# Kernel optimization log

Hardware: AMD Instinct MI355X
Metric: run time of the kernel (lower is better)

## Reference

```python
import jax, jax.numpy as jnp
import numpy as np

D_MODEL = 1024
NUM_HEADS = 16
D_HEAD = D_MODEL // NUM_HEADS
THETA = 10000.0


def _apply_rope(x, pos):
    # x: [B, H, S, Dh]; pos: [S]
    inv_freq = 1.0 / (THETA ** (jnp.arange(0, D_HEAD, 2, dtype=jnp.float32) / D_HEAD))  # [Dh/2]
    freqs = pos[:, None].astype(x.dtype) * inv_freq.astype(x.dtype)  # [S, Dh/2]
    cos = jnp.cos(freqs)  # [S, Dh/2]
    sin = jnp.sin(freqs)
    x1 = x[..., 0::2]  # [B, H, S, Dh/2]
    x2 = x[..., 1::2]
    even = x1 * cos - x2 * sin
    odd = x1 * sin + x2 * cos
    # interleave back: stack on last axis then flatten
    out = jnp.stack([even, odd], axis=-1).reshape(x.shape)
    return out


def setup_inputs() -> dict:
    key = jax.random.key(0)
    k0, k1, k2, k3, k4 = jax.random.split(key, 5)
    B, S = 2, 2048
    scale = 0.02
    return {
        "in_features": jax.random.normal(k0, (B, S, D_MODEL), dtype=jnp.float32),
        "Wq": jax.random.normal(k1, (D_MODEL, D_MODEL), dtype=jnp.float32) * scale,
        "Wk": jax.random.normal(k2, (D_MODEL, D_MODEL), dtype=jnp.float32) * scale,
        "Wv": jax.random.normal(k3, (D_MODEL, D_MODEL), dtype=jnp.float32) * scale,
        "Wo": jax.random.normal(k4, (D_MODEL, D_MODEL), dtype=jnp.float32) * scale,
    }


def reference(in_features, Wq, Wk, Wv, Wo):
    B, S, _ = in_features.shape
    H, Dh = NUM_HEADS, D_HEAD

    def proj(W):
        # torch Linear: y = x @ W^T; split heads -> [B, H, S, Dh]
        y = jnp.einsum('bsd,ed->bse', in_features, W)
        return y.reshape(B, S, H, Dh).transpose(0, 2, 1, 3)

    q = proj(Wq)
    k = proj(Wk)
    v = proj(Wv)

    pos = jnp.arange(S)
    q = _apply_rope(q, pos)
    k = _apply_rope(k, pos)

    scores = jnp.einsum('bhqd,bhkd->bhqk', q, k) / jnp.sqrt(jnp.asarray(Dh, q.dtype))
    causal = jnp.tril(jnp.ones((S, S), dtype=bool))  # True = keep
    scores = jnp.where(causal[None, None, :, :], scores, -jnp.inf)
    att = jax.nn.softmax(scores, axis=-1)
    out = jnp.einsum('bhqk,bhkd->bhqd', att, v)  # [B, H, S, Dh]
    out = out.transpose(0, 2, 1, 3).reshape(B, S, H * Dh)
    return jnp.einsum('bsd,ed->bse', out, Wo)
```

## Files before the change

### kernel.cpp

```cpp
#include <hip/hip_runtime.h>
#include <hip/hip_bf16.h>
#include <math.h>

#define D_MODEL 1024
#define NHEAD 16
#define DHEAD 64
#define SEQ 2048
#define BATCH 2
#define MTOT (BATCH * SEQ)

typedef __attribute__((ext_vector_type(8))) short bf16x8;
typedef __attribute__((ext_vector_type(4))) float f32x4;

static __device__ __forceinline__ ushort f2b(float x) {
  __hip_bfloat16 h = __float2bfloat16(x);
  union { __hip_bfloat16 h; ushort u; } cv; cv.h = h; return cv.u;
}
static __device__ __forceinline__ float b2f(ushort u) {
  union { ushort u; __hip_bfloat16 h; } cv; cv.u = u; return __bfloat162float(cv.h);
}

#define GLLDS16(gp, lp)                                                     \
  __builtin_amdgcn_global_load_lds(                                         \
      (const __attribute__((address_space(1))) unsigned int*)(gp),          \
      (__attribute__((address_space(3))) unsigned int*)(lp), 16, 0, 0)

__global__ __launch_bounds__(256)
void f2b_x(const float* __restrict__ in, ushort* __restrict__ out) {
  int i = blockIdx.x * 256 + threadIdx.x;
  float4 v = ((const float4*)in)[i];
  ushort4 o;
  o.x = f2b(v.x); o.y = f2b(v.y); o.z = f2b(v.z); o.w = f2b(v.w);
  ((ushort4*)out)[i] = o;
}

__global__ __launch_bounds__(256)
void f2b_w4(const float* __restrict__ Wq, const float* __restrict__ Wk,
            const float* __restrict__ Wv, const float* __restrict__ Wo,
            ushort* __restrict__ oq, ushort* __restrict__ ok,
            ushort* __restrict__ ov, ushort* __restrict__ oo) {
  int z = blockIdx.y;
  const float* in = (z == 0) ? Wq : (z == 1) ? Wk : (z == 2) ? Wv : Wo;
  ushort* out = (z == 0) ? oq : (z == 1) ? ok : (z == 2) ? ov : oo;
  int i = blockIdx.x * 256 + threadIdx.x;
  float4 v = ((const float4*)in)[i];
  ushort4 o;
  o.x = f2b(v.x); o.y = f2b(v.y); o.z = f2b(v.z); o.w = f2b(v.w);
  ((ushort4*)out)[i] = o;
}

__global__ __launch_bounds__(256)
void gemm_bf16(const ushort* __restrict__ A,
               const ushort* __restrict__ W0, const ushort* __restrict__ W1,
               const ushort* __restrict__ W2,
               float* __restrict__ outF,
               ushort* __restrict__ o0, ushort* __restrict__ o1,
               ushort* __restrict__ o2, int mode) {
  __shared__ ushort As[128 * 32];
  __shared__ ushort Bs[128 * 32];
  const int tid = threadIdx.x;
  const int lane = tid & 63, w = tid >> 6;
  const int quad = lane >> 4, l15 = lane & 15;
  const int wy = w >> 1, wx = w & 1;
  const int m0 = blockIdx.y * 128, n0 = blockIdx.x * 128;
  const int z = blockIdx.z;
  const ushort* W = (z == 0) ? W0 : (z == 1) ? W1 : W2;
  ushort* outB = (z == 0) ? o0 : (z == 1) ? o1 : o2;

  const int r0 = tid >> 2, c0 = tid & 3;
  const int gc = c0 ^ (r0 & 3);
  const ushort* Ag0 = A + (size_t)(m0 + r0) * D_MODEL + gc * 8;
  const ushort* Ag1 = A + (size_t)(m0 + r0 + 64) * D_MODEL + gc * 8;
  const ushort* Wg0 = W + (size_t)(n0 + r0) * D_MODEL + gc * 8;
  const ushort* Wg1 = W + (size_t)(n0 + r0 + 64) * D_MODEL + gc * 8;

  const int sw = quad ^ (l15 & 3);

  f32x4 acc[4][4];
#pragma unroll
  for (int i = 0; i < 4; ++i)
#pragma unroll
    for (int j = 0; j < 4; ++j) acc[i][j] = (f32x4){0.f, 0.f, 0.f, 0.f};

  for (int kt = 0; kt < D_MODEL / 32; ++kt) {
    if (kt) __syncthreads();
    GLLDS16(Ag0 + kt * 32, &As[(size_t)tid * 8]);
    GLLDS16(Ag1 + kt * 32, &As[(size_t)(tid + 256) * 8]);
    GLLDS16(Wg0 + kt * 32, &Bs[(size_t)tid * 8]);
    GLLDS16(Wg1 + kt * 32, &Bs[(size_t)(tid + 256) * 8]);
    __syncthreads();

    bf16x8 af[4], bfr[4];
#pragma unroll
    for (int mt = 0; mt < 4; ++mt) {
      int row = wy * 64 + mt * 16 + l15;
      af[mt] = *(const bf16x8*)&As[(row * 4 + sw) * 8];
    }
#pragma unroll
    for (int nt = 0; nt < 4; ++nt) {
      int row = wx * 64 + nt * 16 + l15;
      bfr[nt] = *(const bf16x8*)&Bs[(row * 4 + sw) * 8];
    }
#pragma unroll
    for (int mt = 0; mt < 4; ++mt)
#pragma unroll
      for (int nt = 0; nt < 4; ++nt)
        acc[mt][nt] = __builtin_amdgcn_mfma_f32_16x16x32_bf16(
            af[mt], bfr[nt], acc[mt][nt], 0, 0, 0);
  }

#pragma unroll
  for (int mt = 0; mt < 4; ++mt) {
#pragma unroll
    for (int r = 0; r < 4; ++r) {
      int m = m0 + wy * 64 + mt * 16 + quad * 4 + r;
#pragma unroll
      for (int nt = 0; nt < 4; ++nt) {
        int n = n0 + wx * 64 + nt * 16 + l15;
        float v = acc[mt][nt][r];
        if (mode == 0) {
          outF[(size_t)m * D_MODEL + n] = v;
        } else {
          int b = m >> 11, s = m & (SEQ - 1);
          int h = n >> 6, dh = n & 63;
          outB[(((size_t)(b * NHEAD + h)) * SEQ + s) * DHEAD + dh] = f2b(v);
        }
      }
    }
  }
}

__global__ __launch_bounds__(256)
void rope_b(ushort* __restrict__ Q, ushort* __restrict__ K) {
  int p = blockIdx.x * 256 + threadIdx.x;
  ushort* ptr = (blockIdx.y == 0 ? Q : K) + 2 * (size_t)p;
  int i = p & 31;
  int s = (p >> 5) & (SEQ - 1);
  float inv = exp2f((float)i * -0.4152410118609203f);
  float f = (float)s * inv;
  float sn, cs;
  sincosf(f, &sn, &cs);
  uint v = *(uint*)ptr;
  float x1 = b2f((ushort)(v & 0xFFFF));
  float x2 = b2f((ushort)(v >> 16));
  float e = x1 * cs - x2 * sn;
  float o = x1 * sn + x2 * cs;
  *(uint*)ptr = (uint)f2b(e) | ((uint)f2b(o) << 16);
}

__global__ __launch_bounds__(256)
void vtrans(const ushort* __restrict__ V, ushort* __restrict__ Vt) {
  __shared__ ushort T[64][72];
  int bh = blockIdx.y;
  int s0 = blockIdx.x * 64;
  int t = threadIdx.x;
  int r = t >> 2, c4 = t & 3;
  const ushort* src = V + ((size_t)bh * SEQ + s0 + r) * 64 + c4 * 16;
  *(float4*)&T[r][c4 * 16]     = *(const float4*)(src);
  *(float4*)&T[r][c4 * 16 + 8] = *(const float4*)(src + 8);
  __syncthreads();
  union { ushort u[16]; float4 f[2]; } tmp;
#pragma unroll
  for (int j = 0; j < 16; ++j) tmp.u[j] = T[c4 * 16 + j][r];
  ushort* dst = Vt + ((size_t)bh * 64 + r) * SEQ + s0 + c4 * 16;
  *(float4*)dst = tmp.f[0];
  *(float4*)(dst + 8) = tmp.f[1];
}

__global__ __launch_bounds__(256)
void flash_mfma(const ushort* __restrict__ Q, const ushort* __restrict__ K,
                const ushort* __restrict__ Vt, ushort* __restrict__ O) {
  __shared__ ushort Ks[64][72];
  __shared__ ushort Vs[64][72];
  __shared__ ushort Ps[4][16][72];
  const int tid = threadIdx.x;
  const int lane = tid & 63, w = tid >> 6;
  const int quad = lane >> 4, l15 = lane & 15;
  const int h = blockIdx.y, b = blockIdx.z;
  const int qt = (h >= 8) ? (31 - blockIdx.x) : blockIdx.x;
  const int bh = b * NHEAD + h;

  const ushort* Qrow = Q + ((size_t)bh * SEQ + qt * 64 + w * 16 + l15) * 64;
  bf16x8 aq0 = *(const bf16x8*)(Qrow + quad * 8);
  bf16x8 aq1 = *(const bf16x8*)(Qrow + 32 + quad * 8);

  const int sr = tid >> 3, sc8 = (tid & 7) * 8;
  const ushort* Kg0 = K + ((size_t)bh * SEQ + sr) * 64 + sc8;
  const ushort* Kg1 = Kg0 + (size_t)32 * 64;
  const ushort* Vg0 = Vt + ((size_t)bh * 64 + sr) * SEQ + sc8;
  const ushort* Vg1 = Vg0 + (size_t)32 * SEQ;

  float rsl[4];
  f32x4 accO[4];
#pragma unroll
  for (int r = 0; r < 4; ++r) rsl[r] = 0.f;
#pragma unroll
  for (int nt = 0; nt < 4; ++nt) accO[nt] = (f32x4){0.f, 0.f, 0.f, 0.f};

  float4 pk0 = *(const float4*)(Kg0);
  float4 pk1 = *(const float4*)(Kg1);
  float4 pv0 = *(const float4*)(Vg0);
  float4 pv1 = *(const float4*)(Vg1);

  const float SCL = 0.18033688011112042f;
  const int qrow0 = qt * 64 + w * 16 + quad * 4;

  for (int kt = 0; kt <= qt; ++kt) {
    __syncthreads();
    *(float4*)&Ks[sr][sc8]      = pk0;
    *(float4*)&Ks[sr + 32][sc8] = pk1;
    *(float4*)&Vs[sr][sc8]      = pv0;
    *(float4*)&Vs[sr + 32][sc8] = pv1;
    __syncthreads();
    if (kt < qt) {
      pk0 = *(const float4*)(Kg0 + (size_t)(kt + 1) * 64 * 64);
      pk1 = *(const float4*)(Kg1 + (size_t)(kt + 1) * 64 * 64);
      pv0 = *(const float4*)(Vg0 + (kt + 1) * 64);
      pv1 = *(const float4*)(Vg1 + (kt + 1) * 64);
    }

    f32x4 sc[4];
#pragma unroll
    for (int nt = 0; nt < 4; ++nt) {
      bf16x8 bk0 = *(const bf16x8*)&Ks[nt * 16 + l15][quad * 8];
      bf16x8 bk1 = *(const bf16x8*)&Ks[nt * 16 + l15][32 + quad * 8];
      f32x4 zz = (f32x4){0.f, 0.f, 0.f, 0.f};
      zz = __builtin_amdgcn_mfma_f32_16x16x32_bf16(aq0, bk0, zz, 0, 0, 0);
      zz = __builtin_amdgcn_mfma_f32_16x16x32_bf16(aq1, bk1, zz, 0, 0, 0);
      sc[nt] = zz;
    }

    const bool diag = (kt == qt);
#pragma unroll
    for (int nt = 0; nt < 4; ++nt) {
      int kg = kt * 64 + nt * 16 + l15;
#pragma unroll
      for (int r = 0; r < 4; ++r) {
        float p = __builtin_amdgcn_exp2f(sc[nt][r] * SCL);
        if (diag && kg > qrow0 + r) p = 0.f;
        Ps[w][quad * 4 + r][nt * 16 + l15] = f2b(p);
        rsl[r] += p;
      }
    }

    bf16x8 ap0 = *(const bf16x8*)&Ps[w][l15][quad * 8];
    bf16x8 ap1 = *(const bf16x8*)&Ps[w][l15][32 + quad * 8];
#pragma unroll
    for (int nt = 0; nt < 4; ++nt) {
      bf16x8 bv0 = *(const bf16x8*)&Vs[nt * 16 + l15][quad * 8];
      bf16x8 bv1 = *(const bf16x8*)&Vs[nt * 16 + l15][32 + quad * 8];
      accO[nt] = __builtin_amdgcn_mfma_f32_16x16x32_bf16(ap0, bv0, accO[nt], 0, 0, 0);
      accO[nt] = __builtin_amdgcn_mfma_f32_16x16x32_bf16(ap1, bv1, accO[nt], 0, 0, 0);
    }
  }

#pragma unroll
  for (int r = 0; r < 4; ++r) {
#pragma unroll
    for (int off = 1; off < 16; off <<= 1) rsl[r] += __shfl_xor(rsl[r], off);
  }

#pragma unroll
  for (int r = 0; r < 4; ++r) {
    float invl = 1.f / rsl[r];
    int qrow = qt * 64 + w * 16 + quad * 4 + r;
    size_t base = ((size_t)(b * SEQ + qrow)) * D_MODEL + h * 64;
#pragma unroll
    for (int nt = 0; nt < 4; ++nt)
      O[base + nt * 16 + l15] = f2b(accO[nt][r] * invl);
  }
}

extern "C" void kernel_launch(void* const* d_in, const int* in_sizes, int n_in,
                              void* d_out, int out_size, void* d_ws, size_t ws_size,
                              hipStream_t stream) {
  const float* X  = (const float*)d_in[0];
  const float* Wq = (const float*)d_in[1];
  const float* Wk = (const float*)d_in[2];
  const float* Wv = (const float*)d_in[3];
  const float* Wo = (const float*)d_in[4];
  float* out = (float*)d_out;

  ushort* Xb  = (ushort*)d_ws;
  ushort* Wqb = Xb  + (size_t)MTOT * D_MODEL;
  ushort* Wkb = Wqb + (size_t)D_MODEL * D_MODEL;
  ushort* Wvb = Wkb + (size_t)D_MODEL * D_MODEL;
  ushort* Wob = Wvb + (size_t)D_MODEL * D_MODEL;
  ushort* Qw  = Wob + (size_t)D_MODEL * D_MODEL;
  ushort* Kw  = Qw  + (size_t)MTOT * D_MODEL;
  ushort* Vw  = Kw  + (size_t)MTOT * D_MODEL;
  ushort* Vtw = Vw  + (size_t)MTOT * D_MODEL;
  ushort* At  = Vtw + (size_t)MTOT * D_MODEL;

  f2b_x<<<(MTOT * D_MODEL / 4) / 256, 256, 0, stream>>>(X, Xb);
  f2b_w4<<<dim3((D_MODEL * D_MODEL / 4) / 256, 4), 256, 0, stream>>>(
      Wq, Wk, Wv, Wo, Wqb, Wkb, Wvb, Wob);

  gemm_bf16<<<dim3(D_MODEL / 128, MTOT / 128, 3), 256, 0, stream>>>(
      Xb, Wqb, Wkb, Wvb, nullptr, Qw, Kw, Vw, 1);

  int pairs = BATCH * NHEAD * SEQ * (DHEAD / 2);
  rope_b<<<dim3(pairs / 256, 2), 256, 0, stream>>>(Qw, Kw);

  vtrans<<<dim3(SEQ / 64, BATCH * NHEAD), 256, 0, stream>>>(Vw, Vtw);

  flash_mfma<<<dim3(SEQ / 64, NHEAD, BATCH), 256, 0, stream>>>(Qw, Kw, Vtw, At);

  gemm_bf16<<<dim3(D_MODEL / 128, MTOT / 128, 1), 256, 0, stream>>>(
      At, Wob, nullptr, nullptr, out, nullptr, nullptr, nullptr, 0);
}
```

Before: 198.4 us.

## Fuse RoPE and softmax scale into QKV GEMM epilogue, use direct LDS loads in attention

Applies RoPE and the softmax log2 scale to Q and K inside the QKV projection GEMM epilogue, using lane shuffles to pair even and odd columns. This removes the separate rope kernel, which re-read and re-wrote Q and K. The two fp32-to-bf16 conversion kernels are merged into one launch. The flash attention kernel now uses global_load_lds with an XOR-swizzled LDS layout in place of register-prefetched K/V tiles. That removes the register double-buffering, so global loads are no longer overlapped with compute, and the epilogue now does per-element sincos work.

```diff
diff --git a/kernel.cpp b/kernel.cpp
--- a/kernel.cpp
+++ b/kernel.cpp
@@ -16,33 +16,32 @@
   __hip_bfloat16 h = __float2bfloat16(x);
   union { __hip_bfloat16 h; ushort u; } cv; cv.h = h; return cv.u;
 }
-static __device__ __forceinline__ float b2f(ushort u) {
-  union { ushort u; __hip_bfloat16 h; } cv; cv.u = u; return __bfloat162float(cv.h);
-}
 
 #define GLLDS16(gp, lp)                                                     \
   __builtin_amdgcn_global_load_lds(                                         \
       (const __attribute__((address_space(1))) unsigned int*)(gp),          \
       (__attribute__((address_space(3))) unsigned int*)(lp), 16, 0, 0)
 
+#define QSCALE 0.18033688011112042f
+
 __global__ __launch_bounds__(256)
-void f2b_x(const float* __restrict__ in, ushort* __restrict__ out) {
-  int i = blockIdx.x * 256 + threadIdx.x;
-  float4 v = ((const float4*)in)[i];
-  ushort4 o;
-  o.x = f2b(v.x); o.y = f2b(v.y); o.z = f2b(v.z); o.w = f2b(v.w);
-  ((ushort4*)out)[i] = o;
-}
-
-__global__ __launch_bounds__(256)
-void f2b_w4(const float* __restrict__ Wq, const float* __restrict__ Wk,
-            const float* __restrict__ Wv, const float* __restrict__ Wo,
-            ushort* __restrict__ oq, ushort* __restrict__ ok,
-            ushort* __restrict__ ov, ushort* __restrict__ oo) {
-  int z = blockIdx.y;
-  const float* in = (z == 0) ? Wq : (z == 1) ? Wk : (z == 2) ? Wv : Wo;
-  ushort* out = (z == 0) ? oq : (z == 1) ? ok : (z == 2) ? ov : oo;
-  int i = blockIdx.x * 256 + threadIdx.x;
+void f2b_all(const float* __restrict__ X, const float* __restrict__ Wq,
+             const float* __restrict__ Wk, const float* __restrict__ Wv,
+             const float* __restrict__ Wo, ushort* __restrict__ Xb,
+             ushort* __restrict__ Wqb, ushort* __restrict__ Wkb,
+             ushort* __restrict__ Wvb, ushort* __restrict__ Wob) {
+  int bid = blockIdx.x;
+  const float* in;
+  ushort* out;
+  int i;
+  if (bid < 4096) {
+    in = X; out = Xb; i = bid * 256 + threadIdx.x;
+  } else {
+    int ws = (bid - 4096) >> 10;
+    in = (ws == 0) ? Wq : (ws == 1) ? Wk : (ws == 2) ? Wv : Wo;
+    out = (ws == 0) ? Wqb : (ws == 1) ? Wkb : (ws == 2) ? Wvb : Wob;
+    i = ((bid - 4096) & 1023) * 256 + threadIdx.x;
+  }
   float4 v = ((const float4*)in)[i];
   ushort4 o;
   o.x = f2b(v.x); o.y = f2b(v.y); o.z = f2b(v.z); o.w = f2b(v.w);
@@ -59,7 +58,8 @@
   __shared__ ushort As[128 * 32];
   __shared__ ushort Bs[128 * 32];
   const int tid = threadIdx.x;
-  const int lane = tid & 63, w = tid >> 6;
+  const int lane = tid & 63;
+  const int w = tid >> 6;
   const int quad = lane >> 4, l15 = lane & 15;
   const int wy = w >> 1, wx = w & 1;
   const int m0 = blockIdx.y * 128, n0 = blockIdx.x * 128;
@@ -109,11 +109,21 @@
             af[mt], bfr[nt], acc[mt][nt], 0, 0, 0);
   }
 
+  const bool doRope = (mode == 1) && (z < 2);
+  float inv4[4];
+  if (doRope) {
+#pragma unroll
+    for (int nt = 0; nt < 4; ++nt)
+      inv4[nt] = exp2f((float)(nt * 8 + (l15 >> 1)) * -0.4152410118609203f);
+  }
+  const float qsc = (z == 0) ? QSCALE : 1.0f;
+
 #pragma unroll
   for (int mt = 0; mt < 4; ++mt) {
 #pragma unroll
     for (int r = 0; r < 4; ++r) {
       int m = m0 + wy * 64 + mt * 16 + quad * 4 + r;
+      int b = m >> 11, s = m & (SEQ - 1);
 #pragma unroll
       for (int nt = 0; nt < 4; ++nt) {
         int n = n0 + wx * 64 + nt * 16 + l15;
@@ -121,31 +131,23 @@
         if (mode == 0) {
           outF[(size_t)m * D_MODEL + n] = v;
         } else {
-          int b = m >> 11, s = m & (SEQ - 1);
+          if (doRope) {
+            float pv = __shfl_xor(v, 1);
+            float ang = (float)s * inv4[nt];
+            float sn, cs;
+            sincosf(ang, &sn, &cs);
+            bool evn = !(l15 & 1);
+            float x1 = evn ? v : pv;
+            float x2 = evn ? pv : v;
+            v = evn ? (x1 * cs - x2 * sn) : (x1 * sn + x2 * cs);
+            v *= qsc;
+          }
           int h = n >> 6, dh = n & 63;
           outB[(((size_t)(b * NHEAD + h)) * SEQ + s) * DHEAD + dh] = f2b(v);
         }
       }
     }
   }
-}
-
-__global__ __launch_bounds__(256)
-void rope_b(ushort* __restrict__ Q, ushort* __restrict__ K) {
-  int p = blockIdx.x * 256 + threadIdx.x;
-  ushort* ptr = (blockIdx.y == 0 ? Q : K) + 2 * (size_t)p;
-  int i = p & 31;
-  int s = (p >> 5) & (SEQ - 1);
-  float inv = exp2f((float)i * -0.4152410118609203f);
-  float f = (float)s * inv;
-  float sn, cs;
-  sincosf(f, &sn, &cs);
-  uint v = *(uint*)ptr;
-  float x1 = b2f((ushort)(v & 0xFFFF));
-  float x2 = b2f((ushort)(v >> 16));
-  float e = x1 * cs - x2 * sn;
-  float o = x1 * sn + x2 * cs;
-  *(uint*)ptr = (uint)f2b(e) | ((uint)f2b(o) << 16);
 }
 
 __global__ __launch_bounds__(256)
@@ -170,9 +172,9 @@
 __global__ __launch_bounds__(256)
 void flash_mfma(const ushort* __restrict__ Q, const ushort* __restrict__ K,
                 const ushort* __restrict__ Vt, ushort* __restrict__ O) {
-  __shared__ ushort Ks[64][72];
-  __shared__ ushort Vs[64][72];
-  __shared__ ushort Ps[4][16][72];
+  __shared__ ushort Ks[64 * 64];
+  __shared__ ushort Vs[64 * 64];
+  __shared__ ushort Ps[4][16][68];
   const int tid = threadIdx.x;
   const int lane = tid & 63, w = tid >> 6;
   const int quad = lane >> 4, l15 = lane & 15;
@@ -184,11 +186,15 @@
   bf16x8 aq0 = *(const bf16x8*)(Qrow + quad * 8);
   bf16x8 aq1 = *(const bf16x8*)(Qrow + 32 + quad * 8);
 
-  const int sr = tid >> 3, sc8 = (tid & 7) * 8;
-  const ushort* Kg0 = K + ((size_t)bh * SEQ + sr) * 64 + sc8;
-  const ushort* Kg1 = Kg0 + (size_t)32 * 64;
-  const ushort* Vg0 = Vt + ((size_t)bh * 64 + sr) * SEQ + sc8;
-  const ushort* Vg1 = Vg0 + (size_t)32 * SEQ;
+  const int rl = tid >> 3;
+  const int gsc = (tid & 7) ^ (rl & 7);
+  const ushort* Kg  = K  + ((size_t)bh * SEQ + rl) * 64 + gsc * 8;
+  const ushort* Kg2 = Kg + (size_t)32 * 64;
+  const ushort* Vg  = Vt + ((size_t)bh * 64 + rl) * SEQ + gsc * 8;
+  const ushort* Vg2 = Vg + (size_t)32 * SEQ;
+
+  const int sA = (quad ^ (l15 & 7)) * 8;
+  const int sB = sA ^ 32;
 
   float rsl[4];
   f32x4 accO[4];
@@ -197,33 +203,22 @@
 #pragma unroll
   for (int nt = 0; nt < 4; ++nt) accO[nt] = (f32x4){0.f, 0.f, 0.f, 0.f};
 
-  float4 pk0 = *(const float4*)(Kg0);
-  float4 pk1 = *(const float4*)(Kg1);
-  float4 pv0 = *(const float4*)(Vg0);
-  float4 pv1 = *(const float4*)(Vg1);
-
-  const float SCL = 0.18033688011112042f;
   const int qrow0 = qt * 64 + w * 16 + quad * 4;
 
   for (int kt = 0; kt <= qt; ++kt) {
     __syncthreads();
-    *(float4*)&Ks[sr][sc8]      = pk0;
-    *(float4*)&Ks[sr + 32][sc8] = pk1;
-    *(float4*)&Vs[sr][sc8]      = pv0;
-    *(float4*)&Vs[sr + 32][sc8] = pv1;
+    GLLDS16(Kg  + (size_t)kt * 64 * 64, &Ks[tid * 8]);
+    GLLDS16(Kg2 + (size_t)kt * 64 * 64, &Ks[2048 + tid * 8]);
+    GLLDS16(Vg  + kt * 64,              &Vs[tid * 8]);
+    GLLDS16(Vg2 + kt * 64,              &Vs[2048 + tid * 8]);
     __syncthreads();
-    if (kt < qt) {
-      pk0 = *(const float4*)(Kg0 + (size_t)(kt + 1) * 64 * 64);
-      pk1 = *(const float4*)(Kg1 + (size_t)(kt + 1) * 64 * 64);
-      pv0 = *(const float4*)(Vg0 + (kt + 1) * 64);
-      pv1 = *(const float4*)(Vg1 + (kt + 1) * 64);
-    }
 
     f32x4 sc[4];
 #pragma unroll
     for (int nt = 0; nt < 4; ++nt) {
-      bf16x8 bk0 = *(const bf16x8*)&Ks[nt * 16 + l15][quad * 8];
-      bf16x8 bk1 = *(const bf16x8*)&Ks[nt * 16 + l15][32 + quad * 8];
+      const ushort* kr = &Ks[(nt * 16 + l15) * 64];
+      bf16x8 bk0 = *(const bf16x8*)(kr + sA);
+      bf16x8 bk1 = *(const bf16x8*)(kr + sB);
       f32x4 zz = (f32x4){0.f, 0.f, 0.f, 0.f};
       zz = __builtin_amdgcn_mfma_f32_16x16x32_bf16(aq0, bk0, zz, 0, 0, 0);
       zz = __builtin_amdgcn_mfma_f32_16x16x32_bf16(aq1, bk1, zz, 0, 0, 0);
@@ -236,7 +231,7 @@
       int kg = kt * 64 + nt * 16 + l15;
 #pragma unroll
       for (int r = 0; r < 4; ++r) {
-        float p = __builtin_amdgcn_exp2f(sc[nt][r] * SCL);
+        float p = __builtin_amdgcn_exp2f(sc[nt][r]);
         if (diag && kg > qrow0 + r) p = 0.f;
         Ps[w][quad * 4 + r][nt * 16 + l15] = f2b(p);
         rsl[r] += p;
@@ -247,8 +242,9 @@
     bf16x8 ap1 = *(const bf16x8*)&Ps[w][l15][32 + quad * 8];
 #pragma unroll
     for (int nt = 0; nt < 4; ++nt) {
-      bf16x8 bv0 = *(const bf16x8*)&Vs[nt * 16 + l15][quad * 8];
-      bf16x8 bv1 = *(const bf16x8*)&Vs[nt * 16 + l15][32 + quad * 8];
+      const ushort* vr = &Vs[(nt * 16 + l15) * 64];
+      bf16x8 bv0 = *(const bf16x8*)(vr + sA);
+      bf16x8 bv1 = *(const bf16x8*)(vr + sB);
       accO[nt] = __builtin_amdgcn_mfma_f32_16x16x32_bf16(ap0, bv0, accO[nt], 0, 0, 0);
       accO[nt] = __builtin_amdgcn_mfma_f32_16x16x32_bf16(ap1, bv1, accO[nt], 0, 0, 0);
     }
@@ -292,16 +288,11 @@
   ushort* Vtw = Vw  + (size_t)MTOT * D_MODEL;
   ushort* At  = Vtw + (size_t)MTOT * D_MODEL;
 
-  f2b_x<<<(MTOT * D_MODEL / 4) / 256, 256, 0, stream>>>(X, Xb);
-  f2b_w4<<<dim3((D_MODEL * D_MODEL / 4) / 256, 4), 256, 0, stream>>>(
-      Wq, Wk, Wv, Wo, Wqb, Wkb, Wvb, Wob);
+  f2b_all<<<8192, 256, 0, stream>>>(X, Wq, Wk, Wv, Wo, Xb, Wqb, Wkb, Wvb, Wob);
 
   gemm_bf16<<<dim3(D_MODEL / 128, MTOT / 128, 3), 256, 0, stream>>>(
       Xb, Wqb, Wkb, Wvb, nullptr, Qw, Kw, Vw, 1);
 
-  int pairs = BATCH * NHEAD * SEQ * (DHEAD / 2);
-  rope_b<<<dim3(pairs / 256, 2), 256, 0, stream>>>(Qw, Kw);
-
   vtrans<<<dim3(SEQ / 64, BATCH * NHEAD), 256, 0, stream>>>(Vw, Vtw);
 
   flash_mfma<<<dim3(SEQ / 64, NHEAD, BATCH), 256, 0, stream>>>(Qw, Kw, Vtw, At);
```

After: 211.9 us. 1.07x slower.
